# Performance work log

Hardware: AMD Instinct MI355X
Metric: run time of the kernel (lower is better)

## Reference

```python
import jax, jax.numpy as jnp
import numpy as np

SCORE_THRESHOLD = 0.01
NMS_THRESHOLD = 0.5
MAX_DETECTIONS = 100
PRE_NMS_TOPK = 200  # candidates kept per class before NMS (>= MAX_DETECTIONS)


def setup_inputs() -> dict:
    key = jax.random.key(0)
    kc, kcls, kw, kr, kt = jax.random.split(key, 5)
    B, N, C, R = 16, 100000, 30, 3
    # Build valid (x1,y1,x2,y2) boxes: random centers in a 512x512 image, sizes in [1,101].
    cxy = jax.random.uniform(kc, (B, N, 2), dtype=jnp.float32) * 512.0
    wh = jax.random.uniform(kw, (B, N, 2), dtype=jnp.float32) * 100.0 + 1.0
    boxes = jnp.concatenate([cxy - 0.5 * wh, cxy + 0.5 * wh], axis=-1)  # [B,N,4]
    classification = jax.random.uniform(kcls, (B, N, C), dtype=jnp.float32)
    rotation = jax.random.normal(kr, (B, N, R), dtype=jnp.float32)
    translation = jax.random.normal(kt, (B, N, 3), dtype=jnp.float32)
    return {"boxes": boxes, "classification": classification,
            "rotation": rotation, "translation": translation}


def _iou_matrix(b):  # b: [K,4] -> [K,K] pairwise IoU
    x1, y1, x2, y2 = b[:, 0], b[:, 1], b[:, 2], b[:, 3]
    area = jnp.maximum(x2 - x1, 0.0) * jnp.maximum(y2 - y1, 0.0)
    xx1 = jnp.maximum(x1[:, None], x1[None, :])
    yy1 = jnp.maximum(y1[:, None], y1[None, :])
    xx2 = jnp.minimum(x2[:, None], x2[None, :])
    yy2 = jnp.minimum(y2[:, None], y2[None, :])
    inter = jnp.maximum(xx2 - xx1, 0.0) * jnp.maximum(yy2 - yy1, 0.0)
    union = area[:, None] + area[None, :] - inter
    return inter / jnp.maximum(union, 1e-8)


def _nms_one_class(scores, boxes):
    # scores: [N], boxes: [N,4] -> (kept_scores [K], source_indices [K])
    masked = jnp.where(scores > SCORE_THRESHOLD, scores, -jnp.inf)
    top_s, top_i = jax.lax.top_k(masked, PRE_NMS_TOPK)
    cand = boxes[top_i]                      # [K,4], already sorted by score desc
    iou = _iou_matrix(cand)                  # [K,K]
    valid = jnp.isfinite(top_s)
    rng = jnp.arange(PRE_NMS_TOPK)

    def body(i, keep):
        suppress = (iou[i] > NMS_THRESHOLD) & (rng > i) & keep[i]
        return keep & ~suppress

    keep = jax.lax.fori_loop(0, PRE_NMS_TOPK, body, valid)
    return jnp.where(keep, top_s, -jnp.inf), top_i


def reference(boxes, classification, rotation, translation):
    B, N, C = classification.shape

    def per_image(bx, cls, rot, tr):
        # Per-class score threshold + NMS, vectorized over classes.
        s, idx = jax.vmap(lambda c: _nms_one_class(cls[:, c], bx))(jnp.arange(C))
        labels = jnp.broadcast_to(jnp.arange(C)[:, None], s.shape)
        s, idx, labels = s.reshape(-1), idx.reshape(-1), labels.reshape(-1)
        # Global top-k over all (class, kept-box) pairs.
        top_s, sel = jax.lax.top_k(s, MAX_DETECTIONS)
        fidx, flab = idx[sel], labels[sel]
        valid = jnp.isfinite(top_s)
        out_boxes = jnp.where(valid[:, None], bx[fidx], -1.0)
        out_scores = jnp.where(valid, top_s, -1.0)
        out_labels = jnp.where(valid, flab, -1).astype(jnp.int32)
        out_rot = jnp.where(valid[:, None], rot[fidx], -1.0)
        out_tr = jnp.where(valid[:, None], tr[fidx], -1.0)
        return out_boxes, out_scores, out_labels, out_rot, out_tr

    return jax.vmap(per_image)(boxes, classification, rotation, translation)
```

## Files before the change

### kernel.cpp

```cpp
#include <hip/hip_runtime.h>
#include <math.h>

typedef unsigned long long u64;

#define BATCH 16
#define NBOX 100000
#define NCLS 30
#define K 200
#define MAXDET 100
#define SCORE_THR 0.01f
#define NMS_THR 0.5f
#define T0 0.995f

#define ELEM_PER_BATCH (NBOX * NCLS)
#define CAP 1024
#define CHUNKS 48
#define VEC_PER_CHUNK 15625
#define SEG 48
#define OVF 1000000

#define OFF_COLL   0ull
#define OFF_PCNT   (OFF_COLL + (size_t)BATCH*NCLS*CHUNKS*SEG*8)
#define OFF_WSI    (OFF_PCNT + (size_t)BATCH*CHUNKS*32*4)
#define OFF_MERGE  (OFF_WSI + (size_t)BATCH*NCLS*K*4)

__global__ __launch_bounds__(512) void collect_kernel(const float* __restrict__ cls,
                                                      int* __restrict__ pcnt,
                                                      u64* __restrict__ coll) {
  const int b = blockIdx.x / CHUNKS;
  const int chunk = blockIdx.x % CHUNKS;
  const int tid = threadIdx.x;

  __shared__ u64 lbuf[NCLS][SEG];
  __shared__ int lcnt[NCLS];

  if (tid < NCLS) lcnt[tid] = 0;
  __syncthreads();

  const int vbase = chunk * VEC_PER_CHUNK;
  const float4* p = (const float4*)(cls + (size_t)b * ELEM_PER_BATCH) + vbase;

  auto process = [&](float4 v, int idx) {
    float m = fmaxf(fmaxf(v.x, v.y), fmaxf(v.z, v.w));
    if (m > T0) {
      float vv[4] = {v.x, v.y, v.z, v.w};
      #pragma unroll
      for (int j = 0; j < 4; ++j) {
        if (vv[j] > T0) {
          int e = (vbase + idx) * 4 + j;
          int c = e % NCLS;
          int n = e / NCLS;
          int pos = atomicAdd(&lcnt[c], 1);
          if (pos < SEG)
            lbuf[c][pos] = ((u64)__float_as_uint(vv[j]) << 32) | (unsigned)(~(unsigned)n);
        }
      }
    }
  };

  int i = tid;
  for (; i + 1536 < VEC_PER_CHUNK; i += 2048) {
    float4 a  = p[i];
    float4 b2 = p[i + 512];
    float4 c2 = p[i + 1024];
    float4 d2 = p[i + 1536];
    process(a,  i);
    process(b2, i + 512);
    process(c2, i + 1024);
    process(d2, i + 1536);
  }
  for (; i < VEC_PER_CHUNK; i += 512) process(p[i], i);
  __syncthreads();

  if (tid < NCLS) {
    int m = lcnt[tid];
    pcnt[(b * CHUNKS + chunk) * 32 + tid] = (m > SEG) ? OVF : m;
    lcnt[tid] = (m < SEG) ? m : SEG;
  }
  __syncthreads();

  for (int t = tid; t < NCLS * SEG; t += 512) {
    int c = t / SEG, s = t - (t / SEG) * SEG;
    if (s < lcnt[c])
      coll[((size_t)(b * NCLS + c) * CHUNKS + chunk) * SEG + s] = lbuf[c][s];
  }
}

__global__ __launch_bounds__(512) void fused_sort_nms_kernel(
    const u64* __restrict__ coll, const int* __restrict__ pcnt,
    const float* __restrict__ cls, const float* __restrict__ boxes,
    int* __restrict__ ws_i, u64* __restrict__ merged) {
  const int bc = blockIdx.x;
  const int b = bc / NCLS, c = bc % NCLS;
  const int tid = threadIdx.x;

  __shared__ u64 arr[CAP];
  __shared__ float sx1[K], sy1[K], sx2[K], sy2[K], sarea[K], ss[K];
  __shared__ int sidx[K];
  __shared__ unsigned mask[K][8];
  __shared__ unsigned keepw[8];
  __shared__ int s_surv;
  __shared__ u64 comb[256];
  __shared__ unsigned eqbuf[512];
  __shared__ unsigned s_pref, s_mask, s_krem, s_takeall;
  __shared__ unsigned s_cntgt, s_cnteq;
  __shared__ int scnt[CHUNKS], soff[CHUNKS];
  __shared__ int s_total, s_bad;

  if (tid < CHUNKS) scnt[tid] = pcnt[(b * CHUNKS + tid) * 32 + c];
  __syncthreads();
  if (tid == 0) {
    int tot = 0, bad = 0;
    for (int ch = 0; ch < CHUNKS; ++ch) {
      int v = scnt[ch];
      if (v > SEG) bad = 1;
      soff[ch] = tot;
      tot += v;
    }
    if (tot < K || tot > CAP) bad = 1;
    s_total = tot; s_bad = bad;
  }
  __syncthreads();
  const bool bad = (s_bad != 0);

  if (!bad) {
    const int N = (s_total <= 512) ? 512 : CAP;
    for (int i = tid; i < N; i += 512) arr[i] = 0ull;
    __syncthreads();
    for (int t = tid; t < CHUNKS * SEG; t += 512) {
      int ch = t / SEG, s = t - (t / SEG) * SEG;
      if (s < scnt[ch])
        arr[soff[ch] + s] = coll[((size_t)bc * CHUNKS + ch) * SEG + s];
    }
    for (int k = 2; k <= N; k <<= 1) {
      for (int j = k >> 1; j > 0; j >>= 1) {
        __syncthreads();
        for (int i = tid; i < N; i += 512) {
          int l = i ^ j;
          if (l > i) {
            u64 a = arr[i], bb = arr[l];
            bool up = ((i & k) == 0);
            if (up ? (a < bb) : (a > bb)) { arr[i] = bb; arr[l] = a; }
          }
        }
      }
    }
    __syncthreads();
    for (int r = tid; r < K; r += 512) {
      u64 e = arr[r];
      float s = (e != 0ull) ? __uint_as_float((unsigned)(e >> 32)) : -INFINITY;
      int idx = (e != 0ull) ? (int)(~(unsigned)e) : 0;
      ss[r] = s; sidx[r] = idx;
      ws_i[bc * K + r] = idx;
    }
  } else {
    unsigned (*hist)[256] = (unsigned (*)[256])arr;
    const int wv = tid >> 6;
    if (tid == 0) { s_pref = 0u; s_mask = 0u; s_krem = K; s_takeall = 0u; }
    __syncthreads();
    const float* col = cls + (size_t)b * NBOX * NCLS + c;

    for (int pass = 0; pass < 4; ++pass) {
      if (s_takeall) break;
      const int shift = 24 - 8 * pass;
      for (int i = tid; i < 8 * 256; i += 512) ((unsigned*)hist)[i] = 0u;
      __syncthreads();
      const unsigned pref = s_pref, msk = s_mask;
      for (int n = tid; n < NBOX; n += 512) {
        float v = col[(size_t)n * NCLS];
        if (v > SCORE_THR) {
          unsigned key = __float_as_uint(v);
          if ((key & msk) == pref)
            atomicAdd(&hist[wv][(key >> shift) & 0xFFu], 1u);
        }
      }
      __syncthreads();
      if (tid < 256) {
        unsigned t2 = 0;
        for (int w = 0; w < 8; ++w) t2 += hist[w][tid];
        hist[0][tid] = t2;
      }
      __syncthreads();
      if (tid == 0) {
        unsigned krem = s_krem, cum = 0; int dsel = -1;
        for (int d = 255; d >= 0; --d) {
          unsigned cc = hist[0][d];
          if (cum + cc >= krem) { dsel = d; break; }
          cum += cc;
        }
        if (dsel < 0) s_takeall = 1u;
        else {
          s_krem = krem - cum;
          s_pref = pref | ((unsigned)dsel << shift);
          s_mask = msk | (0xFFu << shift);
        }
      }
      __syncthreads();
    }

    if (tid == 0) { s_cntgt = 0u; s_cnteq = 0u; }
    __syncthreads();
    const unsigned pivot = s_pref;
    const unsigned takeall = s_takeall;

    for (int n = tid; n < NBOX; n += 512) {
      float v = col[(size_t)n * NCLS];
      if (v > SCORE_THR) {
        unsigned key = __float_as_uint(v);
        if (takeall || key > pivot) {
          unsigned pos = atomicAdd(&s_cntgt, 1u);
          if (pos < 256u)
            comb[pos] = ((u64)key << 32) | (unsigned)(~(unsigned)n);
        } else if (key == pivot) {
          unsigned pos = atomicAdd(&s_cnteq, 1u);
          if (pos < 512u) eqbuf[pos] = (unsigned)n;
        }
      }
    }
    __syncthreads();
    const unsigned cntgt = (s_cntgt < 256u) ? s_cntgt : 256u;
    const unsigned cnteq = (s_cnteq < 512u) ? s_cnteq : 512u;
    unsigned need = 0;
    if (!takeall) {
      need = (cntgt < (unsigned)K) ? ((unsigned)K - cntgt) : 0u;
      if (need > cnteq) need = cnteq;
    }
    for (int i = tid; i < 512; i += 512)
      if ((unsigned)i >= cnteq) eqbuf[i] = 0xFFFFFFFFu;
    for (int k = 2; k <= 512; k <<= 1) {
      for (int j = k >> 1; j > 0; j >>= 1) {
        __syncthreads();
        {
          int i = tid, l = i ^ j;
          if (l > i) {
            unsigned a = eqbuf[i], bb = eqbuf[l];
            bool up = ((i & k) == 0);
            if (up ? (a > bb) : (a < bb)) { eqbuf[i] = bb; eqbuf[l] = a; }
          }
        }
      }
    }
    __syncthreads();
    for (int t = tid; t < (int)need; t += 512)
      comb[cntgt + t] = ((u64)pivot << 32) | (unsigned)(~eqbuf[t]);
    const unsigned M = cntgt + need;
    for (int i = tid; i < 256; i += 512)
      if ((unsigned)i >= M) comb[i] = 0ull;
    for (int k = 2; k <= 256; k <<= 1) {
      for (int j = k >> 1; j > 0; j >>= 1) {
        __syncthreads();
        if (tid < 256) {
          int i = tid, l = i ^ j;
          if (l > i) {
            u64 a = comb[i], bb = comb[l];
            bool up = ((i & k) == 0);
            if (up ? (a < bb) : (a > bb)) { comb[i] = bb; comb[l] = a; }
          }
        }
      }
    }
    __syncthreads();
    if (tid < K) {
      if ((unsigned)tid < M) {
        u64 e = comb[tid];
        ss[tid] = __uint_as_float((unsigned)(e >> 32));
        sidx[tid] = (int)(~(unsigned)e);
      } else {
        ss[tid] = -INFINITY;
        sidx[tid] = 0;
      }
      ws_i[bc * K + tid] = sidx[tid];
    }
  }
  for (int i = tid; i < K * 8; i += 512) ((unsigned*)mask)[i] = 0u;
  if (tid < 8) keepw[tid] = 0u;
  __syncthreads();

  for (int r = tid; r < K; r += 512) {
    float s = ss[r];
    bool valid = (s != -INFINITY);
    float x1 = 0.f, y1 = 0.f, x2 = 0.f, y2 = 0.f;
    if (valid) {
      const float* bp = boxes + ((size_t)b * NBOX + sidx[r]) * 4;
      x1 = bp[0]; y1 = bp[1]; x2 = bp[2]; y2 = bp[3];
      atomicOr(&keepw[r >> 5], 1u << (r & 31));
    }
    sx1[r] = x1; sy1[r] = y1; sx2[r] = x2; sy2[r] = y2;
    sarea[r] = fmaxf(x2 - x1, 0.f) * fmaxf(y2 - y1, 0.f);
  }
  __syncthreads();

  for (int t = tid; t < K * K; t += 512) {
    int i = t / K, j = t - i * K;
    if (j > i) {
      float xx1 = fmaxf(sx1[i], sx1[j]);
      float yy1 = fmaxf(sy1[i], sy1[j]);
      float xx2 = fminf(sx2[i], sx2[j]);
      float yy2 = fminf(sy2[i], sy2[j]);
      float inter = fmaxf(xx2 - xx1, 0.f) * fmaxf(yy2 - yy1, 0.f);
      float uni = sarea[i] + sarea[j] - inter;
      float iou = inter / fmaxf(uni, 1e-8f);
      if (iou > NMS_THR) atomicOr(&mask[i][j >> 5], 1u << (j & 31));
    }
  }
  __syncthreads();

  if (tid < 64) {
    int w = tid & 7;
    unsigned keep = keepw[w];
    for (int i = 0; i < K; ++i) {
      unsigned kw = __shfl(keep, i >> 5, 64);
      if ((kw >> (i & 31)) & 1u)
        keep &= ~mask[i][w];
    }
    if (tid < 8) keepw[tid] = keep;
  }
  __syncthreads();

  for (int r = tid; r < K; r += 512) {
    int w6 = r >> 5, bit = r & 31;
    if ((keepw[w6] >> bit) & 1u) {
      int pos = 0;
      #pragma unroll
      for (int w = 0; w < 7; ++w) {
        unsigned kw = keepw[w];
        if (w < w6) pos += __popc(kw);
        else if (w == w6) pos += __popc(kw & ((1u << bit) - 1u));
      }
      if (pos < 128) {
        unsigned ord = __float_as_uint(ss[r]) | 0x80000000u;
        merged[((size_t)b * 32 + c) * 128 + pos] =
          ((u64)ord << 32) | (unsigned)(~(unsigned)(c * K + r));
      }
    }
  }
  if (tid == 0) {
    int S = 0;
    #pragma unroll
    for (int w = 0; w < 7; ++w) S += __popc(keepw[w]);
    s_surv = S;
  }
  __syncthreads();
  for (int t = s_surv + tid; t < 128; t += 512)
    merged[((size_t)b * 32 + c) * 128 + t] = 0ull;
}

__device__ __forceinline__ int merge_path_128(const u64* __restrict__ A,
                                              const u64* __restrict__ B, int diag) {
  int lo = 0, hi = diag;
  while (lo < hi) {
    int mid = (lo + hi) >> 1;
    if (A[mid] >= B[diag - 1 - mid]) lo = mid + 1; else hi = mid;
  }
  return lo;
}

__global__ __launch_bounds__(1024) void merge_gather_kernel(
    const u64* __restrict__ merged, const int* __restrict__ ws_i,
    const float* __restrict__ boxes, const float* __restrict__ rot,
    const float* __restrict__ tr, float* __restrict__ out) {
  const int b = blockIdx.x;
  const int tid = threadIdx.x;
  __shared__ u64 S0[32 * 128];
  __shared__ u64 S1[16 * 128];

  for (int t = tid; t < 4096; t += 1024) {
    int c = t >> 7, r = t & 127;
    S0[t] = (c < NCLS) ? merged[((size_t)b * 32 + c) * 128 + r] : 0ull;
  }
  __syncthreads();

  #pragma unroll
  for (int level = 0; level < 5; ++level) {
    const int npairs = 16 >> level;
    const int nout = npairs * 128;
    const u64* src = (level & 1) ? S1 : S0;
    u64* dst = (level & 1) ? S0 : S1;
    for (int t = tid; t < nout; t += 1024) {
      int p = t >> 7, r = t & 127;
      const u64* A = src + (2 * p) * 128;
      const u64* B = src + (2 * p + 1) * 128;
      int i = merge_path_128(A, B, r);
      int j = r - i;
      u64 a = A[i], bb = B[j];
      dst[p * 128 + r] = (a >= bb) ? a : bb;
    }
    __syncthreads();
  }

  if (tid < MAXDET) {
    u64 key = S1[tid];
    bool valid = (key != 0ull);
    float* ob  = out + ((size_t)b * MAXDET + tid) * 4;
    float* os  = out + (size_t)BATCH * MAXDET * 4 + b * MAXDET + tid;
    float* ol  = os + BATCH * MAXDET;
    float* orr = out + (size_t)BATCH * MAXDET * 6 + ((size_t)b * MAXDET + tid) * 3;
    float* ot  = orr + (size_t)BATCH * MAXDET * 3;

    if (valid) {
      unsigned f = ~(unsigned)key;
      int cl = (int)(f / K);
      float sc = __uint_as_float((unsigned)(key >> 32) & 0x7FFFFFFFu);
      int orig = ws_i[(size_t)b * NCLS * K + f];
      const float* bp = boxes + ((size_t)b * NBOX + orig) * 4;
      ob[0] = bp[0]; ob[1] = bp[1]; ob[2] = bp[2]; ob[3] = bp[3];
      *os = sc;
      *ol = (float)cl;
      const float* rp = rot + ((size_t)b * NBOX + orig) * 3;
      orr[0] = rp[0]; orr[1] = rp[1]; orr[2] = rp[2];
      const float* tp = tr + ((size_t)b * NBOX + orig) * 3;
      ot[0] = tp[0]; ot[1] = tp[1]; ot[2] = tp[2];
    } else {
      ob[0] = ob[1] = ob[2] = ob[3] = -1.f;
      *os = -1.f; *ol = -1.f;
      orr[0] = orr[1] = orr[2] = -1.f;
      ot[0] = ot[1] = ot[2] = -1.f;
    }
  }
}

extern "C" void kernel_launch(void* const* d_in, const int* in_sizes, int n_in,
                              void* d_out, int out_size, void* d_ws, size_t ws_size,
                              hipStream_t stream) {
  const float* boxes = (const float*)d_in[0];
  const float* cls   = (const float*)d_in[1];
  const float* rot   = (const float*)d_in[2];
  const float* tr    = (const float*)d_in[3];
  float* out = (float*)d_out;

  char* ws = (char*)d_ws;
  u64*   coll   = (u64*)(ws + OFF_COLL);
  int*   pcnt   = (int*)(ws + OFF_PCNT);
  int*   ws_i   = (int*)(ws + OFF_WSI);
  u64*   merged = (u64*)(ws + OFF_MERGE);

  collect_kernel<<<BATCH * CHUNKS, 512, 0, stream>>>(cls, pcnt, coll);
  fused_sort_nms_kernel<<<BATCH * NCLS, 512, 0, stream>>>(coll, pcnt, cls, boxes,
                                                          ws_i, merged);
  merge_gather_kernel<<<BATCH, 1024, 0, stream>>>(merged, ws_i, boxes, rot, tr, out);
}
```

Before: 103.5 us.

## Replace shared-memory bitonic sort with wave-shuffle sort plus merge-path merges

The full bitonic sort in shared memory, with a barrier per stage, is replaced by two phases. First, 64-element runs are sorted in registers using wavefront shuffles. Then the runs are merged pairwise with a per-thread merge-path binary search, ping-ponging between two shared buffers. This cuts the number of block-wide barriers and shared-memory passes, at the cost of an extra 8KB shared buffer and divergent binary searches.

```diff
diff --git a/kernel.cpp b/kernel.cpp
--- a/kernel.cpp
+++ b/kernel.cpp
@@ -95,6 +95,7 @@
   const int tid = threadIdx.x;
 
   __shared__ u64 arr[CAP];
+  __shared__ u64 arr2[CAP];
   __shared__ float sx1[K], sy1[K], sx2[K], sy2[K], sarea[K], ss[K];
   __shared__ int sidx[K];
   __shared__ unsigned mask[K][8];
@@ -132,22 +133,55 @@
       if (s < scnt[ch])
         arr[soff[ch] + s] = coll[((size_t)bc * CHUNKS + ch) * SEG + s];
     }
-    for (int k = 2; k <= N; k <<= 1) {
-      for (int j = k >> 1; j > 0; j >>= 1) {
-        __syncthreads();
-        for (int i = tid; i < N; i += 512) {
-          int l = i ^ j;
-          if (l > i) {
-            u64 a = arr[i], bb = arr[l];
-            bool up = ((i & k) == 0);
-            if (up ? (a < bb) : (a > bb)) { arr[i] = bb; arr[l] = a; }
+    __syncthreads();
+
+    {
+      const int lane = tid & 63, w = tid >> 6;
+      for (int run = w; run < (N >> 6); run += 8) {
+        u64 v = arr[(run << 6) + lane];
+        #pragma unroll
+        for (int k = 2; k <= 64; k <<= 1) {
+          #pragma unroll
+          for (int j = k >> 1; j > 0; j >>= 1) {
+            u64 o = __shfl_xor(v, j, 64);
+            bool up = ((lane & k) == 0);
+            bool lower = ((lane & j) == 0);
+            u64 mn = (v < o) ? v : o;
+            u64 mx = (v < o) ? o : v;
+            v = (up != lower) ? mn : mx;
           }
         }
-      }
-    }
-    __syncthreads();
+        arr[(run << 6) + lane] = v;
+      }
+    }
+    __syncthreads();
+
+    u64* src = arr;
+    u64* dst = arr2;
+    for (int L = 64; L < N; L <<= 1) {
+      const int twoL = L << 1;
+      for (int t = tid; t < N; t += 512) {
+        int pair = t / twoL;
+        int diag = t - pair * twoL;
+        const u64* A = src + pair * twoL;
+        const u64* B = A + L;
+        int lo = (diag > L) ? (diag - L) : 0;
+        int hi = (diag < L) ? diag : L;
+        while (lo < hi) {
+          int mid = (lo + hi) >> 1;
+          if (A[mid] >= B[diag - 1 - mid]) lo = mid + 1; else hi = mid;
+        }
+        int i2 = lo, j2 = diag - lo;
+        u64 av = (i2 < L) ? A[i2] : 0ull;
+        u64 bv = (j2 < L) ? B[j2] : 0ull;
+        dst[t] = (i2 < L && (j2 >= L || av >= bv)) ? av : bv;
+      }
+      __syncthreads();
+      u64* tmp = src; src = dst; dst = tmp;
+    }
+
     for (int r = tid; r < K; r += 512) {
-      u64 e = arr[r];
+      u64 e = src[r];
       float s = (e != 0ull) ? __uint_as_float((unsigned)(e >> 32)) : -INFINITY;
       int idx = (e != 0ull) ? (int)(~(unsigned)e) : 0;
       ss[r] = s; sidx[r] = idx;
```

Result: faster. 92.98 us (median of 2 runs) (-10.2%).
